# Kernel tuning notes

Measured on AMD Instinct MI355X. Metric: run time of the kernel, lower is better.

The kernel has to match this reference:

```python
import jax, jax.numpy as jnp
import numpy as np


def setup_inputs() -> dict:
    key = jax.random.key(0)
    ks = jax.random.split(key, 7)
    T, D, V = 2048, 1024, 28  # frames, encoder hidden, vocab_size
    s = 0.05  # keras 'random_normal' initializer stddev
    return {
        "x": jax.random.normal(ks[0], (1, T, D), jnp.float32),
        "Wa": jax.random.normal(ks[1], (1, V), jnp.float32) * s,
        "Ua": jax.random.normal(ks[2], (1, D), jnp.float32) * s,
        "Va": jax.random.normal(ks[3], (1, 1), jnp.float32) * s,
        "Wo": jax.random.normal(ks[4], (V, V), jnp.float32) * s,
        "Uo": jax.random.normal(ks[5], (V, D), jnp.float32) * s,
        "Co": jax.random.normal(ks[6], (V, D), jnp.float32) * s,
    }


def reference(x, Wa, Ua, Va, Wo, Uo, Co):
    # Source uses only the first batch element: x = x[0]
    xb = x[0]                      # (T, D)
    V = Wo.shape[0]
    D = Uo.shape[1]
    # Ua . x[j] is constant across outer steps t (source recomputes it; math identical)
    ux = xb @ Ua[0]                # (T,)

    def step(carry, xt):
        Y, H = carry               # Y: (V,) previous output, H: (D,) previous frame
        prev = Wa[0] @ Y           # scalar: Wa . Yanterior
        scores = Va[0, 0] * jnp.tanh(ux + prev)   # (T,)
        # Source applies K.softmax (axis=-1) to scores of shape (T,1,1):
        # softmax over a size-1 axis -> all ones. Reproduced faithfully.
        w = jax.nn.softmax(scores[:, None], axis=-1)   # (T, 1), all ones
        context = (xb * w).sum(axis=0)                 # (D,)
        y = jax.nn.sigmoid(Wo @ Y + Uo @ H + Co @ context)  # (V,)
        return (y, xt), y          # Hanterior <- x[t]

    init = (jnp.zeros((V,), xb.dtype), jnp.zeros((D,), xb.dtype))
    _, ys = jax.lax.scan(step, init, xb)   # ys: (T, V)
    return ys[None]                        # (1, T, V)
```

## Files before the change

kernel.cpp:

```cpp
#include <hip/hip_runtime.h>

#define T_FRAMES 2048
#define D_DIM    1024
#define V_DIM    28
#define BSTRIDE  32
#define LOG2E_F  1.44269504088896f

#define CHUNK    16
#define WARM     24
#define NCHUNK   (T_FRAMES / CHUNK)

#define NB_COL   64
#define NB_PREP  (NB_COL + T_FRAMES)

__global__ __launch_bounds__(256) void prep_kernel(const float* __restrict__ x,
                                                   const float* __restrict__ Uo,
                                                   const float* __restrict__ Co,
                                                   float* __restrict__ cpart,
                                                   float* __restrict__ Bmat) {
    int tid = threadIdx.x;
    __shared__ float xs[D_DIM];

    if (blockIdx.x < NB_COL) {
        int r  = blockIdx.x;
        const float4* xp = (const float4*)(x + (size_t)(r * 32) * D_DIM) + tid;
        float4 s = make_float4(0.f, 0.f, 0.f, 0.f);
#pragma unroll 8
        for (int rr = 0; rr < 32; ++rr) {
            float4 v = xp[rr * (D_DIM / 4)];
            s.x += v.x; s.y += v.y; s.z += v.z; s.w += v.w;
        }
        ((float4*)xs)[tid] = s;
        __syncthreads();

        int wave = tid >> 6, lane = tid & 63;
#pragma unroll
        for (int q = 0; q < 7; ++q) {
            int i = wave * 7 + q;
            const float* crow = Co + (size_t)i * D_DIM;
            float acc = 0.f;
#pragma unroll
            for (int m = 0; m < 16; ++m) {
                int k = lane + 64 * m;
                acc += crow[k] * xs[k];
            }
#pragma unroll
            for (int off = 32; off > 0; off >>= 1) acc += __shfl_down(acc, off);
            if (lane == 0) cpart[(size_t)i * 64 + r] = acc;
        }
        return;
    }

    int t = blockIdx.x - NB_COL;
    if (t == 0) {
        if (tid < BSTRIDE) Bmat[tid] = 0.f;
        return;
    }
    if (tid < 4) Bmat[(size_t)t * BSTRIDE + V_DIM + tid] = 0.f;

    const float* xrow = x + (size_t)(t - 1) * D_DIM;
#pragma unroll
    for (int m = 0; m < 4; ++m) xs[tid + 256 * m] = xrow[tid + 256 * m];
    __syncthreads();

    int wave = tid >> 6, lane = tid & 63;
#pragma unroll
    for (int q = 0; q < 7; ++q) {
        int i = wave * 7 + q;
        const float* urow = Uo + (size_t)i * D_DIM;
        float s = 0.f;
#pragma unroll
        for (int m = 0; m < 16; ++m) {
            int k = lane + 64 * m;
            s += urow[k] * xs[k];
        }
#pragma unroll
        for (int off = 32; off > 0; off >>= 1) s += __shfl_down(s, off);
        if (lane == 0) Bmat[(size_t)t * BSTRIDE + i] = s * LOG2E_F;
    }
}

#define RL(j) __int_as_float(__builtin_amdgcn_readlane(yi_, j))

#define DECL_W(j) float w##j = act ? Wo[(size_t)lane * V_DIM + j] * LOG2E_F : 0.f;
#define REP28(X) X(0) X(1) X(2) X(3) X(4) X(5) X(6) X(7) X(8) X(9) X(10) X(11) \
                 X(12) X(13) X(14) X(15) X(16) X(17) X(18) X(19) X(20) X(21)  \
                 X(22) X(23) X(24) X(25) X(26) X(27)

#define STEP(bval, ydst)                                                     \
    {                                                                        \
        int yi_ = __float_as_int(y);                                         \
        float a0 = (bval) + cik, a1 = 0.f, a2 = 0.f, a3 = 0.f;               \
        a0 = fmaf(w0,  RL(0),  a0);  a1 = fmaf(w1,  RL(1),  a1);             \
        a2 = fmaf(w2,  RL(2),  a2);  a3 = fmaf(w3,  RL(3),  a3);             \
        a0 = fmaf(w4,  RL(4),  a0);  a1 = fmaf(w5,  RL(5),  a1);             \
        a2 = fmaf(w6,  RL(6),  a2);  a3 = fmaf(w7,  RL(7),  a3);             \
        a0 = fmaf(w8,  RL(8),  a0);  a1 = fmaf(w9,  RL(9),  a1);             \
        a2 = fmaf(w10, RL(10), a2);  a3 = fmaf(w11, RL(11), a3);             \
        a0 = fmaf(w12, RL(12), a0);  a1 = fmaf(w13, RL(13), a1);             \
        a2 = fmaf(w14, RL(14), a2);  a3 = fmaf(w15, RL(15), a3);             \
        a0 = fmaf(w16, RL(16), a0);  a1 = fmaf(w17, RL(17), a1);             \
        a2 = fmaf(w18, RL(18), a2);  a3 = fmaf(w19, RL(19), a3);             \
        a0 = fmaf(w20, RL(20), a0);  a1 = fmaf(w21, RL(21), a1);             \
        a2 = fmaf(w22, RL(22), a2);  a3 = fmaf(w23, RL(23), a3);             \
        a0 = fmaf(w24, RL(24), a0);  a1 = fmaf(w25, RL(25), a1);             \
        a2 = fmaf(w26, RL(26), a2);  a3 = fmaf(w27, RL(27), a3);             \
        float acc_ = (a0 + a1) + (a2 + a3);                                  \
        y = __builtin_amdgcn_rcpf(1.f + __builtin_amdgcn_exp2f(-acc_));      \
        ydst = y;                                                            \
    }

#define SSTEP(n)                                                             \
    {                                                                        \
        int tn_ = (t + 1 < T_FRAMES) ? t + 1 : 0;                            \
        float bn_ = Bmat[(size_t)tn_ * BSTRIDE + bl];          \
        STEP(bcur, yb##n)                                                    \
        bcur = bn_; ++t;                                                     \
    }

__global__ __launch_bounds__(64, 1) void scan_kernel(const float* __restrict__ Bmat,
                                                     const float* __restrict__ cpart,
                                                     const float* __restrict__ Wo,
                                                     float* __restrict__ out) {
    int lane = threadIdx.x;
    bool act = lane < V_DIM;
    int bl   = lane & (BSTRIDE - 1);

    REP28(DECL_W)

    const float4* cp4 = (const float4*)(cpart + (size_t)(act ? lane : 0) * 64);
    float cs0 = 0.f, cs1 = 0.f, cs2 = 0.f, cs3 = 0.f;
#pragma unroll
    for (int m = 0; m < 16; m += 4) {
        float4 a = cp4[m],     b = cp4[m + 1];
        float4 e = cp4[m + 2], f = cp4[m + 3];
        cs0 += (a.x + a.y) + (a.z + a.w);
        cs1 += (b.x + b.y) + (b.z + b.w);
        cs2 += (e.x + e.y) + (e.z + e.w);
        cs3 += (f.x + f.y) + (f.z + f.w);
    }
    float cik = act ? ((cs0 + cs1) + (cs2 + cs3)) * LOG2E_F : 0.f;

    int tstore = blockIdx.x * CHUNK;
    int t0     = tstore - WARM; if (t0 < 0) t0 = 0;
    int nwarm  = tstore - t0;

    float y    = 0.f;
    int   t    = t0;
    float bcur = Bmat[(size_t)t0 * BSTRIDE + bl];

    for (int s = 0; s < nwarm; ++s) {
        float bnext = Bmat[(size_t)(t + 1) * BSTRIDE + bl];
        float dump;
        STEP(bcur, dump)
        (void)dump;
        bcur = bnext; ++t;
    }

    float yb0, yb1, yb2, yb3, yb4, yb5, yb6, yb7;
    float yb8, yb9, yb10, yb11, yb12, yb13, yb14, yb15;
    SSTEP(0)  SSTEP(1)  SSTEP(2)  SSTEP(3)
    SSTEP(4)  SSTEP(5)  SSTEP(6)  SSTEP(7)
    SSTEP(8)  SSTEP(9)  SSTEP(10) SSTEP(11)
    SSTEP(12) SSTEP(13) SSTEP(14) SSTEP(15)

    if (act) {
        float* op = out + (size_t)tstore * V_DIM + lane;
        op[0  * V_DIM] = yb0;  op[1  * V_DIM] = yb1;
        op[2  * V_DIM] = yb2;  op[3  * V_DIM] = yb3;
        op[4  * V_DIM] = yb4;  op[5  * V_DIM] = yb5;
        op[6  * V_DIM] = yb6;  op[7  * V_DIM] = yb7;
        op[8  * V_DIM] = yb8;  op[9  * V_DIM] = yb9;
        op[10 * V_DIM] = yb10; op[11 * V_DIM] = yb11;
        op[12 * V_DIM] = yb12; op[13 * V_DIM] = yb13;
        op[14 * V_DIM] = yb14; op[15 * V_DIM] = yb15;
    }
}

extern "C" void kernel_launch(void* const* d_in, const int* in_sizes, int n_in,
                              void* d_out, int out_size, void* d_ws, size_t ws_size,
                              hipStream_t stream) {
    const float* x  = (const float*)d_in[0];
    const float* Wo = (const float*)d_in[4];
    const float* Uo = (const float*)d_in[5];
    const float* Co = (const float*)d_in[6];
    float* out = (float*)d_out;

    float* W     = (float*)d_ws;
    float* cpart = W;
    float* Bmat  = W + 2048;

    prep_kernel<<<NB_PREP, 256, 0, stream>>>(x, Uo, Co, cpart, Bmat);
    scan_kernel<<<NCHUNK,  64,  0, stream>>>(Bmat, cpart, Wo, out);
}
```

Before: 95.51 us.

## Batch eight frames per prep block and keep Uo rows in registers

```diff
diff --git a/kernel.cpp b/kernel.cpp
--- a/kernel.cpp
+++ b/kernel.cpp
@@ -10,74 +10,80 @@
 #define WARM     24
 #define NCHUNK   (T_FRAMES / CHUNK)
 
-#define NB_COL   64
-#define NB_PREP  (NB_COL + T_FRAMES)
+#define RPB      8
+#define NB_PREP  (T_FRAMES / RPB)
 
 __global__ __launch_bounds__(256) void prep_kernel(const float* __restrict__ x,
                                                    const float* __restrict__ Uo,
                                                    const float* __restrict__ Co,
                                                    float* __restrict__ cpart,
                                                    float* __restrict__ Bmat) {
-    int tid = threadIdx.x;
-    __shared__ float xs[D_DIM];
-
-    if (blockIdx.x < NB_COL) {
-        int r  = blockIdx.x;
-        const float4* xp = (const float4*)(x + (size_t)(r * 32) * D_DIM) + tid;
-        float4 s = make_float4(0.f, 0.f, 0.f, 0.f);
-#pragma unroll 8
-        for (int rr = 0; rr < 32; ++rr) {
-            float4 v = xp[rr * (D_DIM / 4)];
-            s.x += v.x; s.y += v.y; s.z += v.z; s.w += v.w;
-        }
-        ((float4*)xs)[tid] = s;
-        __syncthreads();
-
-        int wave = tid >> 6, lane = tid & 63;
-#pragma unroll
-        for (int q = 0; q < 7; ++q) {
-            int i = wave * 7 + q;
-            const float* crow = Co + (size_t)i * D_DIM;
-            float acc = 0.f;
-#pragma unroll
-            for (int m = 0; m < 16; ++m) {
-                int k = lane + 64 * m;
-                acc += crow[k] * xs[k];
-            }
-#pragma unroll
-            for (int off = 32; off > 0; off >>= 1) acc += __shfl_down(acc, off);
-            if (lane == 0) cpart[(size_t)i * 64 + r] = acc;
-        }
-        return;
-    }
-
-    int t = blockIdx.x - NB_COL;
-    if (t == 0) {
-        if (tid < BSTRIDE) Bmat[tid] = 0.f;
-        return;
-    }
-    if (tid < 4) Bmat[(size_t)t * BSTRIDE + V_DIM + tid] = 0.f;
-
-    const float* xrow = x + (size_t)(t - 1) * D_DIM;
-#pragma unroll
-    for (int m = 0; m < 4; ++m) xs[tid + 256 * m] = xrow[tid + 256 * m];
+    int tid = threadIdx.x, b = blockIdx.x;
+    __shared__ float xs[RPB * D_DIM];
+    __shared__ float cs[D_DIM];
+
+    const float4* xb4 = (const float4*)(x + (size_t)b * RPB * D_DIM);
+    float4 csum = make_float4(0.f, 0.f, 0.f, 0.f);
+#pragma unroll
+    for (int r = 0; r < RPB; ++r) {
+        float4 v = xb4[r * (D_DIM / 4) + tid];
+        ((float4*)xs)[r * (D_DIM / 4) + tid] = v;
+        csum.x += v.x; csum.y += v.y; csum.z += v.z; csum.w += v.w;
+    }
+    ((float4*)cs)[tid] = csum;
     __syncthreads();
 
     int wave = tid >> 6, lane = tid & 63;
+
 #pragma unroll
     for (int q = 0; q < 7; ++q) {
         int i = wave * 7 + q;
-        const float* urow = Uo + (size_t)i * D_DIM;
-        float s = 0.f;
-#pragma unroll
-        for (int m = 0; m < 16; ++m) {
-            int k = lane + 64 * m;
-            s += urow[k] * xs[k];
+        const float4* c4 = (const float4*)(Co + (size_t)i * D_DIM);
+        float acc = 0.f;
+#pragma unroll
+        for (int m = 0; m < 4; ++m) {
+            float4 a = c4[lane + 64 * m];
+            float4 d = ((const float4*)cs)[lane + 64 * m];
+            acc += a.x * d.x + a.y * d.y + a.z * d.z + a.w * d.w;
         }
 #pragma unroll
-        for (int off = 32; off > 0; off >>= 1) s += __shfl_down(s, off);
-        if (lane == 0) Bmat[(size_t)t * BSTRIDE + i] = s * LOG2E_F;
-    }
+        for (int off = 32; off > 0; off >>= 1) acc += __shfl_down(acc, off);
+        if (lane == 0) cpart[(size_t)i * NB_PREP + b] = acc;
+    }
+
+    float4 u[7][4];
+#pragma unroll
+    for (int q = 0; q < 7; ++q) {
+        const float4* u4 = (const float4*)(Uo + (size_t)(wave * 7 + q) * D_DIM);
+#pragma unroll
+        for (int m = 0; m < 4; ++m) u[q][m] = u4[lane + 64 * m];
+    }
+
+#pragma unroll
+    for (int r = 0; r < RPB; ++r) {
+        int t = b * RPB + r + 1;
+        if (t >= T_FRAMES) break;
+        float4 xv[4];
+#pragma unroll
+        for (int m = 0; m < 4; ++m)
+            xv[m] = ((const float4*)xs)[r * (D_DIM / 4) + lane + 64 * m];
+#pragma unroll
+        for (int q = 0; q < 7; ++q) {
+            float acc = 0.f;
+#pragma unroll
+            for (int m = 0; m < 4; ++m) {
+                acc = fmaf(u[q][m].x, xv[m].x, acc);
+                acc = fmaf(u[q][m].y, xv[m].y, acc);
+                acc = fmaf(u[q][m].z, xv[m].z, acc);
+                acc = fmaf(u[q][m].w, xv[m].w, acc);
+            }
+#pragma unroll
+            for (int off = 32; off > 0; off >>= 1) acc += __shfl_down(acc, off);
+            if (lane == 0) Bmat[(size_t)t * BSTRIDE + wave * 7 + q] = acc * LOG2E_F;
+        }
+    }
+
+    if (b == 0 && tid < BSTRIDE) Bmat[tid] = 0.f;
 }
 
 #define RL(j) __int_as_float(__builtin_amdgcn_readlane(yi_, j))
@@ -128,16 +134,16 @@
 
     REP28(DECL_W)
 
-    const float4* cp4 = (const float4*)(cpart + (size_t)(act ? lane : 0) * 64);
+    const float4* cp4 = (const float4*)(cpart + (size_t)(act ? lane : 0) * NB_PREP);
     float cs0 = 0.f, cs1 = 0.f, cs2 = 0.f, cs3 = 0.f;
 #pragma unroll
-    for (int m = 0; m < 16; m += 4) {
-        float4 a = cp4[m],     b = cp4[m + 1];
-        float4 e = cp4[m + 2], f = cp4[m + 3];
+    for (int m = 0; m < 64; m += 4) {
+        float4 a = cp4[m],     e = cp4[m + 1];
+        float4 f = cp4[m + 2], g = cp4[m + 3];
         cs0 += (a.x + a.y) + (a.z + a.w);
-        cs1 += (b.x + b.y) + (b.z + b.w);
-        cs2 += (e.x + e.y) + (e.z + e.w);
-        cs3 += (f.x + f.y) + (f.z + f.w);
+        cs1 += (e.x + e.y) + (e.z + e.w);
+        cs2 += (f.x + f.y) + (f.z + f.w);
+        cs3 += (g.x + g.y) + (g.z + g.w);
     }
     float cik = act ? ((cs0 + cs1) + (cs2 + cs3)) * LOG2E_F : 0.f;
 
@@ -188,7 +194,7 @@
 
     float* W     = (float*)d_ws;
     float* cpart = W;
-    float* Bmat  = W + 2048;
+    float* Bmat  = W + 8192;
 
     prep_kernel<<<NB_PREP, 256, 0, stream>>>(x, Uo, Co, cpart, Bmat);
     scan_kernel<<<NCHUNK,  64,  0, stream>>>(Bmat, cpart, Wo, out);
```

After: 103.3 us. +8.2%, slower.
